# Kernel tuning notes

Measured on AMD Instinct MI355X. Metric: run time of the kernel, lower is better.

## Reference

```python
import jax, jax.numpy as jnp
import numpy as np

N_NODES = 50000
N_EDGES = 800000
IN_DIM, HID_DIM, OUT_DIM = 128, 64, 64
NEG_SLOPE = 0.2


def setup_inputs() -> dict:
    key = jax.random.key(0)
    ks = jax.random.split(key, 9)
    return {
        "x": jax.random.normal(ks[0], (N_NODES, IN_DIM), dtype=jnp.float32),
        "edge_index": jax.random.randint(ks[1], (2, N_EDGES), 0, N_NODES, dtype=jnp.int64),
        "W1": jax.random.normal(ks[2], (IN_DIM, HID_DIM), dtype=jnp.float32) * 0.1,
        "a1_src": jax.random.normal(ks[3], (HID_DIM,), dtype=jnp.float32) * 0.1,
        "a1_dst": jax.random.normal(ks[4], (HID_DIM,), dtype=jnp.float32) * 0.1,
        "b1": jnp.zeros((HID_DIM,), dtype=jnp.float32),
        "W2": jax.random.normal(ks[5], (HID_DIM, OUT_DIM), dtype=jnp.float32) * 0.1,
        "a2_src": jax.random.normal(ks[6], (OUT_DIM,), dtype=jnp.float32) * 0.1,
        "a2_dst": jax.random.normal(ks[7], (OUT_DIM,), dtype=jnp.float32) * 0.1,
        "b2": jnp.zeros((OUT_DIM,), dtype=jnp.float32),
    }


def gat_conv(x, src, dst, W, a_src, a_dst, b, n_nodes):
    """Single-head GATConv (PyG semantics, self-loops already appended)."""
    h = x @ W                               # [N, D]
    s_src = h @ a_src                       # [N]
    s_dst = h @ a_dst                       # [N]
    e = s_src[src] + s_dst[dst]             # [E] edge logits
    e = jnp.where(e >= 0, e, NEG_SLOPE * e)  # leaky_relu(0.2)
    # softmax over incoming edges of each destination node (numerically stable)
    m = jax.ops.segment_max(e, dst, num_segments=n_nodes)   # [N]
    e = jnp.exp(e - m[dst])
    denom = jax.ops.segment_sum(e, dst, num_segments=n_nodes)
    alpha = e / denom[dst]                  # [E]
    out = jax.ops.segment_sum(alpha[:, None] * h[src], dst, num_segments=n_nodes)
    return out + b


def reference(x, edge_index, W1, a1_src, a1_dst, b1, W2, a2_src, a2_dst, b2):
    n = x.shape[0]
    loop = jnp.arange(n, dtype=edge_index.dtype)
    src = jnp.concatenate([edge_index[0], loop])  # add self loops (PyG default)
    dst = jnp.concatenate([edge_index[1], loop])
    h = jax.nn.relu(gat_conv(x, src, dst, W1, a1_src, a1_dst, b1, n))
    out = gat_conv(h, src, dst, W2, a2_src, a2_dst, b2, n)
    return out
```

## Files before the change

kernel.cpp:

```cpp
#include <hip/hip_runtime.h>
#include <hip/hip_fp16.h>
#include <type_traits>

#define N_NODES 50000
#define N_EDGES 800000
#define NEG_SLOPE 0.2f
#define NBKT 196
#define EBLK 200
#define CHUNK 4000
#define GEMM_BLOCKS 782

__device__ __forceinline__ float leaky(float x) { return x >= 0.f ? x : NEG_SLOPE * x; }
__device__ __forceinline__ float readlane_f(float v, int i) {
    return __uint_as_float(__builtin_amdgcn_readlane(__float_as_uint(v), i));
}
__device__ __forceinline__ unsigned enc_f(float f) {
    unsigned u = __float_as_uint(f);
    return (int)u < 0 ? ~u : (u | 0x80000000u);
}
__device__ __forceinline__ float dec_f(unsigned e) {
    return __uint_as_float((int)e < 0 ? (e & 0x7FFFFFFFu) : ~e);
}

template <int NL>
__device__ __forceinline__ float salvo(int mysrc, float w64,
                                       const __half* __restrict__ h,
                                       int lane, float acc)
{
    float hv[NL];
    #pragma unroll
    for (int j = 0; j < NL; ++j) {
        int s = __builtin_amdgcn_readlane(mysrc, j);
        hv[j] = __half2float(h[(size_t)s * 64 + lane]);
    }
    #pragma unroll
    for (int j = 0; j < NL; ++j)
        acc += readlane_f(w64, j) * hv[j];
    return acc;
}

template <int K, typename XT>
__device__ __forceinline__ void gemm_body(
    const XT* __restrict__ x, const float* __restrict__ W,
    const float* __restrict__ a_src, const float* __restrict__ a_dst,
    __half* __restrict__ h, float* __restrict__ s_src, float* __restrict__ s_dst,
    float* __restrict__ bmax, unsigned* __restrict__ gmax_enc, int n)
{
    constexpr int BK = 32;
    __shared__ float Wl[BK][64];
    __shared__ float xt[BK][68];
    __shared__ float asl[64], adl[64];
    __shared__ float wm[4];

    int tid = threadIdx.x;
    if (tid < 64) { asl[tid] = a_src[tid]; adl[tid] = a_dst[tid]; }
    int tx = tid & 15, ty = tid >> 4;
    int row0 = blockIdx.x * 64;

    float acc[4][4] = {};

    for (int k0 = 0; k0 < K; k0 += BK) {
        __syncthreads();
        {
            const float4* Wg = (const float4*)&W[(size_t)k0 * 64];
            float4* Ws = (float4*)&Wl[0][0];
            Ws[tid]       = Wg[tid];
            Ws[tid + 256] = Wg[tid + 256];
        }
        #pragma unroll
        for (int it = 0; it < 2; ++it) {
            int idx = tid + it * 256;
            int r = idx >> 3, kq = idx & 7;
            int grow = row0 + r;
            float4 v;
            if constexpr (std::is_same<XT, float>::value) {
                v = (grow < n) ? *(const float4*)&x[(size_t)grow * K + k0 + kq * 4]
                               : make_float4(0.f, 0.f, 0.f, 0.f);
            } else {
                if (grow < n) {
                    uint2 raw = *(const uint2*)&x[(size_t)grow * K + k0 + kq * 4];
                    float2 lo = __half22float2(*(__half2*)&raw.x);
                    float2 hi = __half22float2(*(__half2*)&raw.y);
                    v = make_float4(lo.x, lo.y, hi.x, hi.y);
                } else {
                    v = make_float4(0.f, 0.f, 0.f, 0.f);
                }
            }
            xt[kq * 4 + 0][r] = v.x;
            xt[kq * 4 + 1][r] = v.y;
            xt[kq * 4 + 2][r] = v.z;
            xt[kq * 4 + 3][r] = v.w;
        }
        __syncthreads();

        #pragma unroll
        for (int kk = 0; kk < BK; ++kk) {
            float4 wv = *(const float4*)&Wl[kk][tx * 4];
            float4 xv = *(const float4*)&xt[kk][ty * 4];
            acc[0][0] += xv.x * wv.x; acc[0][1] += xv.x * wv.y; acc[0][2] += xv.x * wv.z; acc[0][3] += xv.x * wv.w;
            acc[1][0] += xv.y * wv.x; acc[1][1] += xv.y * wv.y; acc[1][2] += xv.y * wv.z; acc[1][3] += xv.y * wv.w;
            acc[2][0] += xv.z * wv.x; acc[2][1] += xv.z * wv.y; acc[2][2] += xv.z * wv.z; acc[2][3] += xv.z * wv.w;
            acc[3][0] += xv.w * wv.x; acc[3][1] += xv.w * wv.y; acc[3][2] += xv.w * wv.z; acc[3][3] += xv.w * wv.w;
        }
    }

    float wmax = -INFINITY;
    #pragma unroll
    for (int i = 0; i < 4; ++i) {
        int grow = row0 + ty * 4 + i;
        if (grow < n) {
            __half2 p0 = __floats2half2_rn(acc[i][0], acc[i][1]);
            __half2 p1 = __floats2half2_rn(acc[i][2], acc[i][3]);
            uint2 pk = make_uint2(*(unsigned*)&p0, *(unsigned*)&p1);
            *(uint2*)&h[(size_t)grow * 64 + tx * 4] = pk;
        }
        float s1 = acc[i][0] * asl[tx*4+0] + acc[i][1] * asl[tx*4+1]
                 + acc[i][2] * asl[tx*4+2] + acc[i][3] * asl[tx*4+3];
        float s2 = acc[i][0] * adl[tx*4+0] + acc[i][1] * adl[tx*4+1]
                 + acc[i][2] * adl[tx*4+2] + acc[i][3] * adl[tx*4+3];
        #pragma unroll
        for (int m = 1; m < 16; m <<= 1) {
            s1 += __shfl_xor(s1, m, 64);
            s2 += __shfl_xor(s2, m, 64);
        }
        if (grow < n) wmax = fmaxf(wmax, s1);
        if (tx == 0 && grow < n) { s_src[grow] = s1; s_dst[grow] = s2; }
    }
    wmax = fmaxf(wmax, __shfl_xor(wmax, 16, 64));
    wmax = fmaxf(wmax, __shfl_xor(wmax, 32, 64));
    if ((tid & 63) == 0) wm[tid >> 6] = wmax;
    __syncthreads();
    if (tid == 0) {
        float bm = fmaxf(fmaxf(wm[0], wm[1]), fmaxf(wm[2], wm[3]));
        if (bmax) bmax[blockIdx.x] = bm;
        else      atomicMax(gmax_enc, enc_f(bm));
    }
}

template <int K>
__global__ __launch_bounds__(256) void fused_gemm_p1(
    const float* __restrict__ x, const float* __restrict__ W,
    const float* __restrict__ a_src, const float* __restrict__ a_dst,
    __half* __restrict__ h, float* __restrict__ s_src, float* __restrict__ s_dst,
    float* __restrict__ bmax,
    const int* __restrict__ dst_, int* __restrict__ cnt, int n)
{
    if (blockIdx.x >= GEMM_BLOCKS) {
        __shared__ int bins[NBKT];
        int tid = threadIdx.x, b = blockIdx.x - GEMM_BLOCKS;
        if (tid < NBKT) bins[tid] = 0;
        __syncthreads();
        int e0 = b * CHUNK;
        for (int e = e0 + tid; e < e0 + CHUNK; e += 256)
            atomicAdd(&bins[dst_[e] >> 8], 1);
        __syncthreads();
        if (tid < NBKT) cnt[b * NBKT + tid] = bins[tid];
        return;
    }
    gemm_body<K, float>(x, W, a_src, a_dst, h, s_src, s_dst, bmax, nullptr, n);
}

template <int K>
__global__ __launch_bounds__(256) void gat_gemm_kernel_h(
    const __half* __restrict__ x, const float* __restrict__ W,
    const float* __restrict__ a_src, const float* __restrict__ a_dst,
    __half* __restrict__ h, float* __restrict__ s_src, float* __restrict__ s_dst,
    unsigned* __restrict__ gmax_enc, int n)
{
    gemm_body<K, __half>(x, W, a_src, a_dst, h, s_src, s_dst, nullptr, gmax_enc, n);
}

__global__ __launch_bounds__(256) void p23_fused(
    const int* __restrict__ cnt, int* __restrict__ btot,
    const float* __restrict__ bmax, unsigned* __restrict__ gmaxu,
    const int* __restrict__ src, const int* __restrict__ dst,
    unsigned* __restrict__ bkted)
{
    __shared__ int tmp[256];
    __shared__ int boffL[NBKT];
    __shared__ float fm[4];
    int b = blockIdx.x, tid = threadIdx.x;

    int total = 0, myoff = 0;
    if (tid < NBKT) {
        for (int bp = 0; bp < EBLK; ++bp) {
            int v = cnt[bp * NBKT + tid];
            total += v;
            if (bp < b) myoff += v;
        }
    }
    tmp[tid] = (tid < NBKT) ? total : 0;
    __syncthreads();
    for (int off = 1; off < 256; off <<= 1) {
        int a = (tid >= off) ? tmp[tid - off] : 0;
        __syncthreads();
        tmp[tid] += a;
        __syncthreads();
    }
    if (tid < NBKT) {
        int base = tmp[tid] - total;
        boffL[tid] = base + myoff;
        if (b == 0) btot[tid] = total;
    }
    __syncthreads();

    int e0 = b * CHUNK;
    for (int e = e0 + tid; e < e0 + CHUNK; e += 256) {
        int d = dst[e], s = src[e];
        int pos = atomicAdd(&boffL[d >> 8], 1);
        bkted[pos] = ((unsigned)(d & 255) << 16) | (unsigned)s;
    }

    if (b == 0) {
        float m = -INFINITY;
        for (int i = tid; i < GEMM_BLOCKS; i += 256) m = fmaxf(m, bmax[i]);
        #pragma unroll
        for (int off = 32; off; off >>= 1) m = fmaxf(m, __shfl_xor(m, off, 64));
        if ((tid & 63) == 0) fm[tid >> 6] = m;
        __syncthreads();
        if (tid == 0) {
            gmaxu[0] = enc_f(fmaxf(fmaxf(fm[0], fm[1]), fmaxf(fm[2], fm[3])));
            gmaxu[1] = 0;
        }
    }
}

__global__ __launch_bounds__(256) void p4_csr(
    const unsigned* __restrict__ bkted, const int* __restrict__ btot,
    int* __restrict__ row_off, int* __restrict__ csr_src)
{
    __shared__ int tmp[256];
    __shared__ int cur[256];
    __shared__ int s_beg, s_end;
    int j = blockIdx.x, tid = threadIdx.x;
    int v = (tid < NBKT) ? btot[tid] : 0;
    tmp[tid] = v; __syncthreads();
    for (int off = 1; off < 256; off <<= 1) {
        int a = (tid >= off) ? tmp[tid - off] : 0;
        __syncthreads();
        tmp[tid] += a;
        __syncthreads();
    }
    if (tid == j) { s_beg = tmp[tid] - v; s_end = tmp[tid]; }
    cur[tid] = 0;
    __syncthreads();
    int beg = s_beg, end = s_end;

    for (int e = beg + tid; e < end; e += 256)
        atomicAdd(&cur[bkted[e] >> 16], 1);
    __syncthreads();
    int c = cur[tid];
    tmp[tid] = c; __syncthreads();
    for (int off = 1; off < 256; off <<= 1) {
        int a = (tid >= off) ? tmp[tid - off] : 0;
        __syncthreads();
        tmp[tid] += a;
        __syncthreads();
    }
    int offx = tmp[tid] - c;
    int node = j * 256 + tid;
    if (node < N_NODES) row_off[node] = beg + offx;
    if (node == 0) row_off[N_NODES] = N_EDGES;
    __syncthreads();
    cur[tid] = offx;
    __syncthreads();
    for (int e = beg + tid; e < end; e += 256) {
        unsigned u = bkted[e];
        int pos = beg + atomicAdd(&cur[u >> 16], 1);
        csr_src[pos] = (int)(u & 0xFFFFu);
    }
}

template <bool RELU, typename OT>
__global__ __launch_bounds__(256) void gat_node_kernel(
    const int* __restrict__ row_off, const int* __restrict__ csr_src,
    const float* __restrict__ s_src, const float* __restrict__ s_dst,
    const __half* __restrict__ h, const float* __restrict__ b,
    const unsigned* __restrict__ gmax_enc, OT* __restrict__ out, int n)
{
    int row = blockIdx.x * 4 + (threadIdx.x >> 6);
    int lane = threadIdx.x & 63;
    if (row >= n) return;

    int beg = row_off[row], end = row_off[row + 1];
    int deg = end - beg;
    float sd = s_dst[row];
    float m = leaky(dec_f(*gmax_enc) + sd);
    float s_self = s_src[row];
    float hself = __half2float(h[(size_t)row * 64 + lane]);
    float wself = __expf(leaky(s_self + sd) - m);

    float v;
    if (deg <= 32) {
        int mysrc = row;
        if (lane < deg) mysrc = csr_src[beg + lane];
        float my_s = s_src[mysrc];
        float mylogit = (lane < deg) ? leaky(my_s + sd) : -INFINITY;
        float w64 = __expf(mylogit - m);
        float den = w64;
        #pragma unroll
        for (int off = 32; off; off >>= 1)
            den += __shfl_xor(den, off, 64);
        den += wself;

        float acc = wself * hself;
        if (deg <= 16) acc = salvo<16>(mysrc, w64, h, lane, acc);
        else           acc = salvo<32>(mysrc, w64, h, lane, acc);
        v = acc / den + b[lane];
    } else {
        int   mysrc   = row;
        float mylogit = -INFINITY;
        if (lane < deg) {
            mysrc = csr_src[beg + lane];
            mylogit = leaky(s_src[mysrc] + sd);
        }
        float w64 = __expf(mylogit - m);
        float den = w64;
        #pragma unroll
        for (int off = 32; off; off >>= 1)
            den += __shfl_xor(den, off, 64);
        den += wself;

        float acc = wself * hself;
        int d0 = deg < 64 ? deg : 64;
        int nb = (d0 + 15) & ~15;
        for (int i = 0; i < nb; i += 16) {
            float hv[16];
            #pragma unroll
            for (int j = 0; j < 16; ++j) {
                int s = __builtin_amdgcn_readlane(mysrc, i + j);
                hv[j] = __half2float(h[(size_t)s * 64 + lane]);
            }
            #pragma unroll
            for (int j = 0; j < 16; ++j)
                acc += readlane_f(w64, i + j) * hv[j];
        }
        for (int e = beg + 64; e < end; ++e) {
            int s = csr_src[e];
            float w = __expf(leaky(s_src[s] + sd) - m);
            den += w;
            acc += w * __half2float(h[(size_t)s * 64 + lane]);
        }
        v = acc / den + b[lane];
    }

    if (RELU) v = fmaxf(v, 0.f);
    if constexpr (std::is_same<OT, __half>::value)
        out[(size_t)row * 64 + lane] = __float2half(v);
    else
        out[(size_t)row * 64 + lane] = v;
}

extern "C" void kernel_launch(void* const* d_in, const int* in_sizes, int n_in,
                              void* d_out, int out_size, void* d_ws, size_t ws_size,
                              hipStream_t stream) {
    const float* x   = (const float*)d_in[0];
    const int*   ei  = (const int*)d_in[1];
    const float* W1  = (const float*)d_in[2];
    const float* a1s = (const float*)d_in[3];
    const float* a1d = (const float*)d_in[4];
    const float* b1  = (const float*)d_in[5];
    const float* W2  = (const float*)d_in[6];
    const float* a2s = (const float*)d_in[7];
    const float* a2d = (const float*)d_in[8];
    const float* b2  = (const float*)d_in[9];
    float* out = (float*)d_out;

    const int* src = ei;
    const int* dst = ei + N_EDGES;

    char* p = (char*)d_ws;
    __half* h    = (__half*)p;          p += (size_t)N_NODES * 64 * 2;
    __half* outh = (__half*)p;          p += (size_t)N_NODES * 64 * 2;
    float* ssrc = (float*)p;            p += (size_t)N_NODES * 4;
    float* sdst = (float*)p;            p += (size_t)N_NODES * 4;
    int* row_off = (int*)p;             p += (size_t)(N_NODES + 1) * 4;
    unsigned* gmaxu = (unsigned*)p;     p += 4 * 4;
    float* bmax = (float*)p;            p += 1024 * 4;
    int* csr_src = (int*)p;             p += (size_t)N_EDGES * 4;
    int* cnt     = (int*)p;             p += (size_t)EBLK * NBKT * 4;
    int* btot    = (int*)p;             p += (size_t)NBKT * 4;
    unsigned* bkted = (unsigned*)p;     p += (size_t)N_EDGES * 4;

    dim3 blk(256);
    int node_blocks = (N_NODES + 3) / 4;

    fused_gemm_p1<128><<<GEMM_BLOCKS + EBLK, blk, 0, stream>>>(
        x, W1, a1s, a1d, h, ssrc, sdst, bmax, dst, cnt, N_NODES);
    p23_fused<<<EBLK, blk, 0, stream>>>(cnt, btot, bmax, gmaxu, src, dst, bkted);
    p4_csr<<<NBKT, blk, 0, stream>>>(bkted, btot, row_off, csr_src);
    gat_node_kernel<true, __half><<<node_blocks, blk, 0, stream>>>(
        row_off, csr_src, ssrc, sdst, h, b1, gmaxu + 0, outh, N_NODES);
    gat_gemm_kernel_h<64><<<GEMM_BLOCKS, blk, 0, stream>>>(
        outh, W2, a2s, a2d, h, ssrc, sdst, gmaxu + 1, N_NODES);
    gat_node_kernel<false, float><<<node_blocks, blk, 0, stream>>>(
        row_off, csr_src, ssrc, sdst, h, b2, gmaxu + 1, out, N_NODES);
}
```

Measured before the change: 122.3 us.

## Use bf16 MFMA for first-layer GEMM in fused kernel

Replaces the scalar FP32 register-tiled GEMM for layer 1 (K=128) with a bf16 MFMA 16x16x32 path. The whole x tile and W are converted to bf16 in shared memory, and each wave computes 16 rows by 64 columns. The epilogue then computes the attention scores and block max from the MFMA accumulator layout. This cuts FP32 FMA work in the first GEMM, but input precision drops to bf16 and the shared-memory footprint grows.

```diff
diff --git a/kernel.cpp b/kernel.cpp
--- a/kernel.cpp
+++ b/kernel.cpp
@@ -10,6 +10,9 @@
 #define CHUNK 4000
 #define GEMM_BLOCKS 782
 
+typedef __attribute__((ext_vector_type(8))) short short8v;
+typedef __attribute__((ext_vector_type(4))) float f32x4;
+
 __device__ __forceinline__ float leaky(float x) { return x >= 0.f ? x : NEG_SLOPE * x; }
 __device__ __forceinline__ float readlane_f(float v, int i) {
     return __uint_as_float(__builtin_amdgcn_readlane(__float_as_uint(v), i));
@@ -20,6 +23,11 @@
 }
 __device__ __forceinline__ float dec_f(unsigned e) {
     return __uint_as_float((int)e < 0 ? (e & 0x7FFFFFFFu) : ~e);
+}
+__device__ __forceinline__ unsigned short f2bf_bits(float f) {
+    unsigned u = __float_as_uint(f);
+    unsigned r = u + 0x7FFFu + ((u >> 16) & 1u);
+    return (unsigned short)(r >> 16);
 }
 
 template <int NL>
@@ -39,12 +47,117 @@
     return acc;
 }
 
-template <int K, typename XT>
-__device__ __forceinline__ void gemm_body(
-    const XT* __restrict__ x, const float* __restrict__ W,
+__global__ __launch_bounds__(256) void fused_gemm1_p1(
+    const float* __restrict__ x, const float* __restrict__ W,
     const float* __restrict__ a_src, const float* __restrict__ a_dst,
     __half* __restrict__ h, float* __restrict__ s_src, float* __restrict__ s_dst,
-    float* __restrict__ bmax, unsigned* __restrict__ gmax_enc, int n)
+    float* __restrict__ bmax,
+    const int* __restrict__ dst_, int* __restrict__ cnt, int n)
+{
+    if (blockIdx.x >= GEMM_BLOCKS) {
+        __shared__ int bins[NBKT];
+        int tid = threadIdx.x, b = blockIdx.x - GEMM_BLOCKS;
+        if (tid < NBKT) bins[tid] = 0;
+        __syncthreads();
+        int e0 = b * CHUNK;
+        for (int e = e0 + tid; e < e0 + CHUNK; e += 256)
+            atomicAdd(&bins[dst_[e] >> 8], 1);
+        __syncthreads();
+        if (tid < NBKT) cnt[b * NBKT + tid] = bins[tid];
+        return;
+    }
+
+    __shared__ unsigned short xb[64][136];
+    __shared__ unsigned short wb[64][136];
+    __shared__ float asl[64], adl[64];
+    __shared__ float wm[4];
+
+    int tid = threadIdx.x;
+    int row0 = blockIdx.x * 64;
+    if (tid < 64) { asl[tid] = a_src[tid]; adl[tid] = a_dst[tid]; }
+
+    #pragma unroll
+    for (int it = 0; it < 8; ++it) {
+        int idx = tid + it * 256;
+        int r = idx >> 5;
+        int kq = idx & 31;
+        int grow = row0 + r;
+        float4 v = (grow < n) ? ((const float4*)x)[(size_t)grow * 32 + kq]
+                              : make_float4(0.f, 0.f, 0.f, 0.f);
+        xb[r][kq * 4 + 0] = f2bf_bits(v.x);
+        xb[r][kq * 4 + 1] = f2bf_bits(v.y);
+        xb[r][kq * 4 + 2] = f2bf_bits(v.z);
+        xb[r][kq * 4 + 3] = f2bf_bits(v.w);
+    }
+    #pragma unroll
+    for (int it = 0; it < 8; ++it) {
+        int idx = tid + it * 256;
+        int k  = idx >> 4;
+        int cq = idx & 15;
+        float4 v = ((const float4*)W)[idx];
+        wb[cq * 4 + 0][k] = f2bf_bits(v.x);
+        wb[cq * 4 + 1][k] = f2bf_bits(v.y);
+        wb[cq * 4 + 2][k] = f2bf_bits(v.z);
+        wb[cq * 4 + 3][k] = f2bf_bits(v.w);
+    }
+    __syncthreads();
+
+    int wv = tid >> 6, l = tid & 63;
+    int rsub = l & 15;
+    int kg = l >> 4;
+
+    f32x4 acc0 = (f32x4)0.f, acc1 = (f32x4)0.f, acc2c = (f32x4)0.f, acc3 = (f32x4)0.f;
+    #pragma unroll
+    for (int ks = 0; ks < 4; ++ks) {
+        int kb = ks * 32 + kg * 8;
+        short8v a = *(const short8v*)&xb[wv * 16 + rsub][kb];
+        short8v b0 = *(const short8v*)&wb[ 0 + rsub][kb];
+        short8v b1 = *(const short8v*)&wb[16 + rsub][kb];
+        short8v b2 = *(const short8v*)&wb[32 + rsub][kb];
+        short8v b3 = *(const short8v*)&wb[48 + rsub][kb];
+        acc0  = __builtin_amdgcn_mfma_f32_16x16x32_bf16(a, b0, acc0,  0, 0, 0);
+        acc1  = __builtin_amdgcn_mfma_f32_16x16x32_bf16(a, b1, acc1,  0, 0, 0);
+        acc2c = __builtin_amdgcn_mfma_f32_16x16x32_bf16(a, b2, acc2c, 0, 0, 0);
+        acc3  = __builtin_amdgcn_mfma_f32_16x16x32_bf16(a, b3, acc3,  0, 0, 0);
+    }
+
+    float wmax = -INFINITY;
+    #pragma unroll
+    for (int r = 0; r < 4; ++r) {
+        int grow = row0 + wv * 16 + kg * 4 + r;
+        float v0 = acc0[r], v1 = acc1[r], v2 = acc2c[r], v3 = acc3[r];
+        if (grow < n) {
+            h[(size_t)grow * 64 + rsub +  0] = __float2half(v0);
+            h[(size_t)grow * 64 + rsub + 16] = __float2half(v1);
+            h[(size_t)grow * 64 + rsub + 32] = __float2half(v2);
+            h[(size_t)grow * 64 + rsub + 48] = __float2half(v3);
+        }
+        float s1 = v0 * asl[rsub] + v1 * asl[rsub + 16] + v2 * asl[rsub + 32] + v3 * asl[rsub + 48];
+        float s2 = v0 * adl[rsub] + v1 * adl[rsub + 16] + v2 * adl[rsub + 32] + v3 * adl[rsub + 48];
+        #pragma unroll
+        for (int mk = 1; mk < 16; mk <<= 1) {
+            s1 += __shfl_xor(s1, mk, 64);
+            s2 += __shfl_xor(s2, mk, 64);
+        }
+        if (grow < n) {
+            if (rsub == 0) { s_src[grow] = s1; s_dst[grow] = s2; }
+            wmax = fmaxf(wmax, s1);
+        }
+    }
+    wmax = fmaxf(wmax, __shfl_xor(wmax, 16, 64));
+    wmax = fmaxf(wmax, __shfl_xor(wmax, 32, 64));
+    if (l == 0) wm[wv] = wmax;
+    __syncthreads();
+    if (tid == 0)
+        bmax[blockIdx.x] = fmaxf(fmaxf(wm[0], wm[1]), fmaxf(wm[2], wm[3]));
+}
+
+template <int K>
+__global__ __launch_bounds__(256) void gat_gemm_kernel_h(
+    const __half* __restrict__ x, const float* __restrict__ W,
+    const float* __restrict__ a_src, const float* __restrict__ a_dst,
+    __half* __restrict__ h, float* __restrict__ s_src, float* __restrict__ s_dst,
+    unsigned* __restrict__ gmax_enc, int n)
 {
     constexpr int BK = 32;
     __shared__ float Wl[BK][64];
@@ -73,18 +186,13 @@
             int r = idx >> 3, kq = idx & 7;
             int grow = row0 + r;
             float4 v;
-            if constexpr (std::is_same<XT, float>::value) {
-                v = (grow < n) ? *(const float4*)&x[(size_t)grow * K + k0 + kq * 4]
-                               : make_float4(0.f, 0.f, 0.f, 0.f);
+            if (grow < n) {
+                uint2 raw = *(const uint2*)&x[(size_t)grow * K + k0 + kq * 4];
+                float2 lo = __half22float2(*(__half2*)&raw.x);
+                float2 hi = __half22float2(*(__half2*)&raw.y);
+                v = make_float4(lo.x, lo.y, hi.x, hi.y);
             } else {
-                if (grow < n) {
-                    uint2 raw = *(const uint2*)&x[(size_t)grow * K + k0 + kq * 4];
-                    float2 lo = __half22float2(*(__half2*)&raw.x);
-                    float2 hi = __half22float2(*(__half2*)&raw.y);
-                    v = make_float4(lo.x, lo.y, hi.x, hi.y);
-                } else {
-                    v = make_float4(0.f, 0.f, 0.f, 0.f);
-                }
+                v = make_float4(0.f, 0.f, 0.f, 0.f);
             }
             xt[kq * 4 + 0][r] = v.x;
             xt[kq * 4 + 1][r] = v.y;
@@ -132,42 +240,8 @@
     __syncthreads();
     if (tid == 0) {
         float bm = fmaxf(fmaxf(wm[0], wm[1]), fmaxf(wm[2], wm[3]));
-        if (bmax) bmax[blockIdx.x] = bm;
-        else      atomicMax(gmax_enc, enc_f(bm));
-    }
-}
-
-template <int K>
-__global__ __launch_bounds__(256) void fused_gemm_p1(
-    const float* __restrict__ x, const float* __restrict__ W,
-    const float* __restrict__ a_src, const float* __restrict__ a_dst,
-    __half* __restrict__ h, float* __restrict__ s_src, float* __restrict__ s_dst,
-    float* __restrict__ bmax,
-    const int* __restrict__ dst_, int* __restrict__ cnt, int n)
-{
-    if (blockIdx.x >= GEMM_BLOCKS) {
-        __shared__ int bins[NBKT];
-        int tid = threadIdx.x, b = blockIdx.x - GEMM_BLOCKS;
-        if (tid < NBKT) bins[tid] = 0;
-        __syncthreads();
-        int e0 = b * CHUNK;
-        for (int e = e0 + tid; e < e0 + CHUNK; e += 256)
-            atomicAdd(&bins[dst_[e] >> 8], 1);
-        __syncthreads();
-        if (tid < NBKT) cnt[b * NBKT + tid] = bins[tid];
-        return;
-    }
-    gemm_body<K, float>(x, W, a_src, a_dst, h, s_src, s_dst, bmax, nullptr, n);
-}
-
-template <int K>
-__global__ __launch_bounds__(256) void gat_gemm_kernel_h(
-    const __half* __restrict__ x, const float* __restrict__ W,
-    const float* __restrict__ a_src, const float* __restrict__ a_dst,
-    __half* __restrict__ h, float* __restrict__ s_src, float* __restrict__ s_dst,
-    unsigned* __restrict__ gmax_enc, int n)
-{
-    gemm_body<K, __half>(x, W, a_src, a_dst, h, s_src, s_dst, nullptr, gmax_enc, n);
+        atomicMax(gmax_enc, enc_f(bm));
+    }
 }
 
 __global__ __launch_bounds__(256) void p23_fused(
@@ -385,7 +459,7 @@
     dim3 blk(256);
     int node_blocks = (N_NODES + 3) / 4;
 
-    fused_gemm_p1<128><<<GEMM_BLOCKS + EBLK, blk, 0, stream>>>(
+    fused_gemm1_p1<<<GEMM_BLOCKS + EBLK, blk, 0, stream>>>(
         x, W1, a1s, a1d, h, ssrc, sdst, bmax, dst, cnt, N_NODES);
     p23_fused<<<EBLK, blk, 0, stream>>>(cnt, btot, bmax, gmaxu, src, dst, bkted);
     p4_csr<<<NBKT, blk, 0, stream>>>(bkted, btot, row_off, csr_src);
```

Result: faster. 116.5 us (-4.7%).
